# Kernel optimization log

Hardware: AMD Instinct MI355X
Metric: run time of the kernel (lower is better)

Reference implementation:

```python
import jax, jax.numpy as jnp
import numpy as np

B, S, D = 1, 4096, 2048
H, G = 16, 4            # num_heads, kv_group
HD = D // H             # head_dim = 128
GS = H // G             # group_size = 4
THETA = 10000.0


def _rope_params():
    inv_freq = 1.0 / (THETA ** (np.arange(0, HD, 2, dtype=np.float32) / HD))
    ang = np.arange(S, dtype=np.float32)[:, None] * inv_freq[None, :]   # [S, HD/2]
    ang = np.concatenate([ang, ang], axis=1)                             # [S, HD]
    return jnp.asarray(np.cos(ang), jnp.float32), jnp.asarray(np.sin(ang), jnp.float32)


def setup_inputs() -> dict:
    key = jax.random.key(0)
    ks = jax.random.split(key, 5)
    sd = D ** -0.5
    x = jax.random.normal(ks[0], (B, S, D), jnp.float32)
    wq = jax.random.normal(ks[1], (D, D), jnp.float32) * sd
    wk = jax.random.normal(ks[2], (D, G * HD), jnp.float32) * sd
    wv = jax.random.normal(ks[3], (D, G * HD), jnp.float32) * sd
    wo = jax.random.normal(ks[4], (D, D), jnp.float32) * sd
    cos, sin = _rope_params()
    mask = jnp.triu(jnp.ones((S, S), dtype=bool), k=1)  # True = masked (causal)
    return {"x": x, "mask": mask, "wq": wq, "wk": wk, "wv": wv,
            "wo": wo, "cos": cos, "sin": sin}


def _apply_rope(t, cos, sin):
    # t: [b, h, s, hd]
    half = t.shape[-1] // 2
    t1, t2 = t[..., :half], t[..., half:]
    rot = jnp.concatenate([-t2, t1], axis=-1)
    s = t.shape[2]
    return t * cos[None, None, :s, :] + rot * sin[None, None, :s, :]


def reference(x, mask, wq, wk, wv, wo, cos, sin):
    b, s, d = x.shape
    q = (x @ wq).reshape(b, s, H, HD).transpose(0, 2, 1, 3)   # [b,H,s,hd]
    k = (x @ wk).reshape(b, s, G, HD).transpose(0, 2, 1, 3)   # [b,G,s,hd]
    v = (x @ wv).reshape(b, s, G, HD).transpose(0, 2, 1, 3)   # [b,G,s,hd]
    q = _apply_rope(q, cos, sin)
    k = _apply_rope(k, cos, sin)
    # GQA: broadcast K/V over group_size instead of repeat_interleave (same math)
    q = q.reshape(b, G, GS, s, HD)
    scores = jnp.einsum('bgrsd,bgtd->bgrst', q, k)            # [b,G,GS,s,s]
    scores = jnp.where(mask[None, None, None], -jnp.inf, scores)
    w = jax.nn.softmax(scores / jnp.sqrt(jnp.float32(HD)), axis=-1)
    ctx = jnp.einsum('bgrst,bgtd->bgrsd', w, v)               # [b,G,GS,s,hd]
    ctx = ctx.reshape(b, H, s, HD).transpose(0, 2, 1, 3).reshape(b, s, d)
    return ctx @ wo
```

## Files before the change

### kernel.cpp

```cpp
#include <hip/hip_runtime.h>
#include <cstdint>

#define Ssz 4096
#define Dsz 2048
#define Hn  16
#define Gn  4
#define HDn 128

typedef __attribute__((ext_vector_type(8))) short short8;
typedef __attribute__((ext_vector_type(8))) unsigned short u16x8;
typedef __attribute__((ext_vector_type(4))) float f32x4;

typedef __attribute__((address_space(1))) void gbl_void;
typedef __attribute__((address_space(3))) void lds_void;

static __device__ __forceinline__ unsigned short f2bf(float f) {
  uint32_t u = __builtin_bit_cast(uint32_t, f);
  u += 0x7FFFu + ((u >> 16) & 1u);
  return (unsigned short)(u >> 16);
}

static __device__ __forceinline__ void gload_lds16(const void* g, void* l) {
  __builtin_amdgcn_global_load_lds((gbl_void*)(uintptr_t)g,
                                   (lds_void*)(uintptr_t)l, 16, 0, 0);
}

__global__ void k_cast_bf16(const float* __restrict__ src,
                            unsigned short* __restrict__ dst, int n) {
  int base = (blockIdx.x * blockDim.x + threadIdx.x) * 8;
  if (base >= n) return;
  float4 a = *reinterpret_cast<const float4*>(src + base);
  float4 b = *reinterpret_cast<const float4*>(src + base + 4);
  u16x8 o;
  o[0] = f2bf(a.x); o[1] = f2bf(a.y); o[2] = f2bf(a.z); o[3] = f2bf(a.w);
  o[4] = f2bf(b.x); o[5] = f2bf(b.y); o[6] = f2bf(b.z); o[7] = f2bf(b.w);
  *reinterpret_cast<u16x8*>(dst + base) = o;
}

__global__ void k_transpose(const float* __restrict__ src, int srcStride,
                            unsigned short* __restrict__ dst, int dstStride,
                            int R, int C) {
  __shared__ unsigned short tile[64][65];
  const int r0 = blockIdx.y * 64, c0 = blockIdx.x * 64;
  const int t  = threadIdx.x;
  const int rr = t >> 2;
  const int cc = (t & 3) * 16;
  const float* sp = src + (size_t)(r0 + rr) * srcStride + c0 + cc;
#pragma unroll
  for (int j = 0; j < 16; j += 4) {
    float4 v = *reinterpret_cast<const float4*>(sp + j);
    tile[rr][cc + j + 0] = f2bf(v.x);
    tile[rr][cc + j + 1] = f2bf(v.y);
    tile[rr][cc + j + 2] = f2bf(v.z);
    tile[rr][cc + j + 3] = f2bf(v.w);
  }
  __syncthreads();
  unsigned short* dp = dst + (size_t)(c0 + rr) * dstStride + r0 + cc;
  u16x8 o0, o1;
#pragma unroll
  for (int j = 0; j < 8; j++) o0[j] = tile[cc + j][rr];
#pragma unroll
  for (int j = 0; j < 8; j++) o1[j] = tile[cc + 8 + j][rr];
  *reinterpret_cast<u16x8*>(dp)     = o0;
  *reinterpret_cast<u16x8*>(dp + 8) = o1;
}

__global__ void k_rope(const float* __restrict__ Cqkv,
                       const float* __restrict__ cosp, const float* __restrict__ sinp,
                       unsigned short* __restrict__ Qb, unsigned short* __restrict__ Kb) {
  const int s = blockIdx.x;
  const float* row = Cqkv + (size_t)s * 3072;
  const float qscale = 0.08838834764831845f;
  for (int c = threadIdx.x; c < 2560; c += 256) {
    int d = c & 127;
    float v = row[c];
    int pc = (d < 64) ? c + 64 : c - 64;
    float pv = row[pc];
    float rot = (d < 64) ? -pv : pv;
    float o = v * cosp[s * 128 + d] + rot * sinp[s * 128 + d];
    if (c < 2048)
      Qb[(size_t)s * 2048 + c] = f2bf(o * qscale);
    else
      Kb[(size_t)s * 512 + (c - 2048)] = f2bf(o);
  }
}

__global__ __launch_bounds__(256) void k_gemm_bt(
    const unsigned short* __restrict__ A, const unsigned short* __restrict__ BT,
    float* __restrict__ C, int M, int N, int K, int ldc) {
  __shared__ __align__(16) unsigned short sA[128 * 32];
  __shared__ __align__(16) unsigned short sB[128 * 32];
  const int tid = threadIdx.x;
  const int lane = tid & 63, wid = tid >> 6;
  const int m0 = blockIdx.y * 128, n0 = blockIdx.x * 128;
  const int wm = (wid >> 1) * 64, wn = (wid & 1) * 64;
  const int l15 = lane & 15, lg = lane >> 4;
  const int srow = lane >> 2;
  const int scol = (lane & 3) * 8;

  f32x4 acc[4][4] = {};

  for (int kt = 0; kt < K; kt += 32) {
#pragma unroll
    for (int c = 0; c < 2; c++) {
      const int row = c * 64 + wid * 16;
      gload_lds16(A  + (size_t)(m0 + row + srow) * K + kt + scol, sA + row * 32);
      gload_lds16(BT + (size_t)(n0 + row + srow) * K + kt + scol, sB + row * 32);
    }
    __syncthreads();
    short8 af[4], bf[4];
#pragma unroll
    for (int i = 0; i < 4; i++) {
      af[i] = *reinterpret_cast<const short8*>(sA + (wm + i * 16 + l15) * 32 + lg * 8);
      bf[i] = *reinterpret_cast<const short8*>(sB + (wn + i * 16 + l15) * 32 + lg * 8);
    }
#pragma unroll
    for (int i = 0; i < 4; i++)
#pragma unroll
      for (int j = 0; j < 4; j++)
        acc[i][j] = __builtin_amdgcn_mfma_f32_16x16x32_bf16(af[i], bf[j], acc[i][j], 0, 0, 0);
    __syncthreads();
  }

  const int rbase = m0 + wm + lg * 4;
  const int cbase = n0 + wn + l15;
#pragma unroll
  for (int i = 0; i < 4; i++)
#pragma unroll
    for (int j = 0; j < 4; j++)
#pragma unroll
      for (int r = 0; r < 4; r++)
        C[(size_t)(rbase + i * 16 + r) * ldc + cbase + j * 16] = acc[i][j][r];
}

__global__ __launch_bounds__(512, 4) void k_attn(
    const unsigned short* __restrict__ Qb, const unsigned short* __restrict__ Kb,
    const unsigned short* __restrict__ Vt, unsigned short* __restrict__ ctx) {
  __shared__ __align__(16) char sK[2][16384];
  __shared__ __align__(16) char sV[2][16384];
  __shared__ __align__(16) char sP[8][2048];
  const int id = blockIdx.x;
  const int kid = id & 255;
  const int h = kid & 15, g = h >> 2;
  const int j = kid >> 4;
  const int qt = (id < 256) ? (31 - j) : j;
  const int qb = qt * 128;
  const int lane = threadIdx.x & 63, wid = threadIdx.x >> 6;
  const int l15 = lane & 15, lg = lane >> 4;
  const int sw = (l15 & 7) << 4;
  const int wmin = qb + wid * 16;
  const int nt = qt * 2 + 2;

  const char* kbyte = (const char*)Kb;
  const char* vbyte = (const char*)Vt;
  int kOff[2], vOff[2];
#pragma unroll
  for (int q = 0; q < 2; q++) {
    int rk = wid * 8 + q * 4 + (lane >> 4);
    kOff[q] = rk * 1024 + g * 256 + (((lane & 15) * 16) ^ ((rk & 7) << 4));
    int rv = wid * 16 + q * 8 + (lane >> 3);
    vOff[q] = (g * 128 + rv) * 8192 + (((lane & 7) * 16) ^ ((rv & 7) << 4));
  }

  auto stage = [&](int t, int b) {
    const char* ks = kbyte + (size_t)t * 65536;
    const char* vs = vbyte + (size_t)t * 128;
#pragma unroll
    for (int q = 0; q < 2; q++)
      gload_lds16(ks + kOff[q], &sK[b][(wid * 2 + q) * 1024]);
#pragma unroll
    for (int q = 0; q < 2; q++)
      gload_lds16(vs + vOff[q], &sV[b][(wid * 2 + q) * 1024]);
  };

  short8 qf[4];
  {
    const unsigned short* qp = Qb + (size_t)(wmin + l15) * Dsz + h * HDn + lg * 8;
#pragma unroll
    for (int kk = 0; kk < 4; kk++)
      qf[kk] = *reinterpret_cast<const short8*>(qp + kk * 32);
  }

  f32x4 o[8] = {};
  float mrow[4], lrow[4];
#pragma unroll
  for (int r = 0; r < 4; r++) { mrow[r] = -1e30f; lrow[r] = 0.f; }

  stage(0, 0);
  int cur = 0;

  for (int t = 0; t < nt; t++) {
    asm volatile("s_waitcnt vmcnt(0)" ::: "memory");
    __syncthreads();
    if (t + 1 < nt) stage(t + 1, cur ^ 1);
    const int kv0 = t * 64;
    if (kv0 <= wmin + 15) {
      f32x4 sc[4] = {};
#pragma unroll
      for (int f = 0; f < 4; f++) {
        const char* kr = &sK[cur][(f * 16 + l15) * 256];
#pragma unroll
        for (int kk = 0; kk < 4; kk++) {
          short8 kf = *reinterpret_cast<const short8*>(kr + ((kk * 64 + lg * 16) ^ sw));
          sc[f] = __builtin_amdgcn_mfma_f32_16x16x32_bf16(qf[kk], kf, sc[f], 0, 0, 0);
        }
      }
      if (kv0 + 63 > wmin) {
#pragma unroll
        for (int f = 0; f < 4; f++) {
          int kv = kv0 + f * 16 + l15;
#pragma unroll
          for (int r = 0; r < 4; r++)
            if (kv > wmin + lg * 4 + r) sc[f][r] = -1e30f;
        }
      }
      float mx[4], rs[4];
#pragma unroll
      for (int r = 0; r < 4; r++)
        mx[r] = fmaxf(fmaxf(sc[0][r], sc[1][r]), fmaxf(sc[2][r], sc[3][r]));
#pragma unroll
      for (int off = 1; off < 16; off <<= 1)
#pragma unroll
        for (int r = 0; r < 4; r++) mx[r] = fmaxf(mx[r], __shfl_xor(mx[r], off));
      bool grow = false;
#pragma unroll
      for (int r = 0; r < 4; r++) grow = grow || (mx[r] > mrow[r] + 8.f);
      if (__any(grow)) {
#pragma unroll
        for (int r = 0; r < 4; r++) {
          float mn = fmaxf(mrow[r], mx[r]);
          float scale = __expf(mrow[r] - mn);
          mrow[r] = mn;
          lrow[r] *= scale;
#pragma unroll
          for (int nf = 0; nf < 8; nf++) o[nf][r] *= scale;
        }
      }
#pragma unroll
      for (int f = 0; f < 4; f++)
#pragma unroll
        for (int r = 0; r < 4; r++) sc[f][r] = __expf(sc[f][r] - mrow[r]);
#pragma unroll
      for (int r = 0; r < 4; r++)
        rs[r] = sc[0][r] + sc[1][r] + sc[2][r] + sc[3][r];
#pragma unroll
      for (int off = 1; off < 16; off <<= 1)
#pragma unroll
        for (int r = 0; r < 4; r++) rs[r] += __shfl_xor(rs[r], off);
#pragma unroll
      for (int r = 0; r < 4; r++) lrow[r] += rs[r];

      char* plw = &sP[wid][0];
#pragma unroll
      for (int f = 0; f < 4; f++)
#pragma unroll
        for (int r = 0; r < 4; r++) {
          int row = lg * 4 + r;
          *reinterpret_cast<unsigned short*>(
              plw + row * 128 + ((f * 32 + l15 * 2) ^ ((row & 7) << 4))) =
              f2bf(sc[f][r]);
        }
      short8 pa[2];
#pragma unroll
      for (int kk = 0; kk < 2; kk++)
        pa[kk] = *reinterpret_cast<const short8*>(
            plw + l15 * 128 + ((kk * 64 + lg * 16) ^ sw));
#pragma unroll
      for (int nf = 0; nf < 8; nf++) {
        const char* vr = &sV[cur][(nf * 16 + l15) * 128];
#pragma unroll
        for (int kk = 0; kk < 2; kk++) {
          short8 vb = *reinterpret_cast<const short8*>(vr + ((kk * 64 + lg * 16) ^ sw));
          o[nf] = __builtin_amdgcn_mfma_f32_16x16x32_bf16(pa[kk], vb, o[nf], 0, 0, 0);
        }
      }
    }
    cur ^= 1;
  }

  unsigned short* cp = ctx + (size_t)(wmin + lg * 4) * Dsz + h * HDn + l15;
#pragma unroll
  for (int nf = 0; nf < 8; nf++)
#pragma unroll
    for (int r = 0; r < 4; r++)
      cp[(size_t)r * Dsz + nf * 16] = f2bf(o[nf][r] / lrow[r]);
}

extern "C" void kernel_launch(void* const* d_in, const int* in_sizes, int n_in,
                              void* d_out, int out_size, void* d_ws, size_t ws_size,
                              hipStream_t stream) {
  (void)in_sizes; (void)n_in; (void)out_size; (void)ws_size;
  const float* x  = (const float*)d_in[0];
  const float* wq = (const float*)d_in[2];
  const float* wk = (const float*)d_in[3];
  const float* wv = (const float*)d_in[4];
  const float* wo = (const float*)d_in[5];
  const float* cs = (const float*)d_in[6];
  const float* sn = (const float*)d_in[7];
  float* out = (float*)d_out;

  unsigned short* ws16  = (unsigned short*)d_ws;
  unsigned short* WTqkv = ws16;
  unsigned short* WTo   = WTqkv + 3072 * 2048;
  unsigned short* xb    = WTo   + 2048 * 2048;
  unsigned short* Qb    = xb    + 4096 * 2048;
  unsigned short* Kb    = Qb    + 4096 * 2048;
  unsigned short* Vt    = Kb    + 4096 * 512;
  unsigned short* ctx   = Vt    + 512 * 4096;
  float* Cqkv = (float*)(ctx + 4096 * 2048);

  k_cast_bf16<<<4096, 256, 0, stream>>>(x, xb, 4096 * 2048);
  k_transpose<<<dim3(32, 32), 256, 0, stream>>>(wq, 2048, WTqkv,              2048, 2048, 2048);
  k_transpose<<<dim3(8, 32),  256, 0, stream>>>(wk, 512,  WTqkv + 2048 * 2048, 2048, 2048, 512);
  k_transpose<<<dim3(8, 32),  256, 0, stream>>>(wv, 512,  WTqkv + 2560 * 2048, 2048, 2048, 512);
  k_transpose<<<dim3(32, 32), 256, 0, stream>>>(wo, 2048, WTo,                2048, 2048, 2048);

  k_gemm_bt<<<dim3(24, 32), 256, 0, stream>>>(xb, WTqkv, Cqkv, 4096, 3072, 2048, 3072);
  k_rope<<<4096, 256, 0, stream>>>(Cqkv, cs, sn, Qb, Kb);
  k_transpose<<<dim3(8, 64), 256, 0, stream>>>(Cqkv + 2560, 3072, Vt, 4096, 4096, 512);

  k_attn<<<dim3(512), 512, 0, stream>>>(Qb, Kb, Vt, ctx);

  k_gemm_bt<<<dim3(16, 32), 256, 0, stream>>>(ctx, WTo, out, 4096, 2048, 2048, 2048);
}
```

Before: 476.9 us.

## Transpose QK^T MFMA so each lane owns one query row; swizzle GEMM blocks

The attention kernel swaps the MFMA operands so the score tile is laid out transposed. Each lane then holds four key scores for a single query row, so the row max and row sum need only two cross-lane shuffles instead of four rounds over four rows. P is written to LDS as packed 8-byte stores rather than scalar 2-byte stores. Per-row rescale factors and the final normalizer are fetched with shuffles to match the O layout. Separately, the GEMM remaps block IDs across eight groups (an XCD-style swizzle) to improve L2 locality, which assumes the block count divides evenly by eight.

```diff
diff --git a/kernel.cpp b/kernel.cpp
--- a/kernel.cpp
+++ b/kernel.cpp
@@ -92,7 +92,10 @@
   __shared__ __align__(16) unsigned short sB[128 * 32];
   const int tid = threadIdx.x;
   const int lane = tid & 63, wid = tid >> 6;
-  const int m0 = blockIdx.y * 128, n0 = blockIdx.x * 128;
+  const int bid = blockIdx.y * gridDim.x + blockIdx.x;
+  const int cpx = (gridDim.x * gridDim.y) >> 3;
+  const int swz = (bid & 7) * cpx + (bid >> 3);
+  const int m0 = (swz / gridDim.x) * 128, n0 = (swz % gridDim.x) * 128;
   const int wm = (wid >> 1) * 64, wn = (wid & 1) * 64;
   const int l15 = lane & 15, lg = lane >> 4;
   const int srow = lane >> 2;
@@ -182,9 +185,7 @@
   }
 
   f32x4 o[8] = {};
-  float mrow[4], lrow[4];
-#pragma unroll
-  for (int r = 0; r < 4; r++) { mrow[r] = -1e30f; lrow[r] = 0.f; }
+  float mrow_s = -1e30f, lrow_s = 0.f;
 
   stage(0, 0);
   int cur = 0;
@@ -202,64 +203,60 @@
 #pragma unroll
         for (int kk = 0; kk < 4; kk++) {
           short8 kf = *reinterpret_cast<const short8*>(kr + ((kk * 64 + lg * 16) ^ sw));
-          sc[f] = __builtin_amdgcn_mfma_f32_16x16x32_bf16(qf[kk], kf, sc[f], 0, 0, 0);
+          sc[f] = __builtin_amdgcn_mfma_f32_16x16x32_bf16(kf, qf[kk], sc[f], 0, 0, 0);
         }
       }
       if (kv0 + 63 > wmin) {
+        const int qa = wmin + l15;
 #pragma unroll
         for (int f = 0; f < 4; f++) {
-          int kv = kv0 + f * 16 + l15;
+          int kv = kv0 + f * 16 + lg * 4;
 #pragma unroll
           for (int r = 0; r < 4; r++)
-            if (kv > wmin + lg * 4 + r) sc[f][r] = -1e30f;
+            if (kv + r > qa) sc[f][r] = -1e30f;
         }
       }
-      float mx[4], rs[4];
-#pragma unroll
-      for (int r = 0; r < 4; r++)
-        mx[r] = fmaxf(fmaxf(sc[0][r], sc[1][r]), fmaxf(sc[2][r], sc[3][r]));
-#pragma unroll
-      for (int off = 1; off < 16; off <<= 1)
-#pragma unroll
-        for (int r = 0; r < 4; r++) mx[r] = fmaxf(mx[r], __shfl_xor(mx[r], off));
-      bool grow = false;
-#pragma unroll
-      for (int r = 0; r < 4; r++) grow = grow || (mx[r] > mrow[r] + 8.f);
-      if (__any(grow)) {
-#pragma unroll
-        for (int r = 0; r < 4; r++) {
-          float mn = fmaxf(mrow[r], mx[r]);
-          float scale = __expf(mrow[r] - mn);
-          mrow[r] = mn;
-          lrow[r] *= scale;
-#pragma unroll
-          for (int nf = 0; nf < 8; nf++) o[nf][r] *= scale;
-        }
-      }
+      float mx = sc[0][0];
 #pragma unroll
       for (int f = 0; f < 4; f++)
 #pragma unroll
-        for (int r = 0; r < 4; r++) sc[f][r] = __expf(sc[f][r] - mrow[r]);
-#pragma unroll
-      for (int r = 0; r < 4; r++)
-        rs[r] = sc[0][r] + sc[1][r] + sc[2][r] + sc[3][r];
-#pragma unroll
-      for (int off = 1; off < 16; off <<= 1)
-#pragma unroll
-        for (int r = 0; r < 4; r++) rs[r] += __shfl_xor(rs[r], off);
-#pragma unroll
-      for (int r = 0; r < 4; r++) lrow[r] += rs[r];
+        for (int r = 0; r < 4; r++) mx = fmaxf(mx, sc[f][r]);
+      mx = fmaxf(mx, __shfl_xor(mx, 16));
+      mx = fmaxf(mx, __shfl_xor(mx, 32));
+      if (__any(mx > mrow_s + 8.f)) {
+        float mn = fmaxf(mrow_s, mx);
+        float scl = __expf(mrow_s - mn);
+        mrow_s = mn;
+        lrow_s *= scl;
+        float s4[4];
+#pragma unroll
+        for (int r = 0; r < 4; r++)
+          s4[r] = __shfl(scl, (lane & 48) | (lg * 4 + r));
+#pragma unroll
+        for (int nf = 0; nf < 8; nf++)
+#pragma unroll
+          for (int r = 0; r < 4; r++) o[nf][r] *= s4[r];
+      }
+#pragma unroll
+      for (int f = 0; f < 4; f++)
+#pragma unroll
+        for (int r = 0; r < 4; r++) sc[f][r] = __expf(sc[f][r] - mrow_s);
+      float rs = 0.f;
+#pragma unroll
+      for (int f = 0; f < 4; f++)
+        rs += (sc[f][0] + sc[f][1]) + (sc[f][2] + sc[f][3]);
+      rs += __shfl_xor(rs, 16);
+      rs += __shfl_xor(rs, 32);
+      lrow_s += rs;
 
       char* plw = &sP[wid][0];
 #pragma unroll
-      for (int f = 0; f < 4; f++)
-#pragma unroll
-        for (int r = 0; r < 4; r++) {
-          int row = lg * 4 + r;
-          *reinterpret_cast<unsigned short*>(
-              plw + row * 128 + ((f * 32 + l15 * 2) ^ ((row & 7) << 4))) =
-              f2bf(sc[f][r]);
-        }
+      for (int f = 0; f < 4; f++) {
+        uint32_t w0 = (uint32_t)f2bf(sc[f][0]) | ((uint32_t)f2bf(sc[f][1]) << 16);
+        uint32_t w1 = (uint32_t)f2bf(sc[f][2]) | ((uint32_t)f2bf(sc[f][3]) << 16);
+        *reinterpret_cast<uint2*>(plw + l15 * 128 + ((f * 32 + lg * 8) ^ sw)) =
+            make_uint2(w0, w1);
+      }
       short8 pa[2];
 #pragma unroll
       for (int kk = 0; kk < 2; kk++)
@@ -278,12 +275,16 @@
     cur ^= 1;
   }
 
+  float lr4[4];
+#pragma unroll
+  for (int r = 0; r < 4; r++)
+    lr4[r] = __shfl(lrow_s, (lane & 48) | (lg * 4 + r));
   unsigned short* cp = ctx + (size_t)(wmin + lg * 4) * Dsz + h * HDn + l15;
 #pragma unroll
   for (int nf = 0; nf < 8; nf++)
 #pragma unroll
     for (int r = 0; r < 4; r++)
-      cp[(size_t)r * Dsz + nf * 16] = f2bf(o[nf][r] / lrow[r]);
+      cp[(size_t)r * Dsz + nf * 16] = f2bf(o[nf][r] / lr4[r]);
 }
 
 extern "C" void kernel_launch(void* const* d_in, const int* in_sizes, int n_in,
```

Measured after the change: 416.7 us. 1.14x faster.
